# Performance work log

Measured on AMD Instinct MI355X. Metric: run time of the kernel, lower is better.

The kernel has to match this reference:

```python
import jax, jax.numpy as jnp
import numpy as np

B, R, C = 2, 64, 256
PH = PW = 7
KMAX = 8            # max pool-kernel size per axis given roi size bounds (kernel<=7 here)
HW = [160, 80, 40, 20]   # FPN level spatial sizes for a 640px image, strides 4/8/16/32
STRIDES = [4.0, 8.0, 16.0, 32.0]
TOP = 224.0         # config.top_pyramid_roi_size
HIDDEN = 2048
NCLS = 20
SCALE = float(np.round(np.sqrt(C), 2))  # np.round(sqrt(inner_dim),2) in SelfAttention


def setup_inputs() -> dict:
    key = jax.random.key(0)
    ks = jax.random.split(key, 32)
    U = lambda k, s, lo, hi: jax.random.uniform(k, s, minval=lo, maxval=hi)
    x1 = U(ks[0], (B, R), 0.0, 260.0)
    y1 = U(ks[1], (B, R), 0.0, 260.0)
    w = U(ks[2], (B, R), 16.0, 360.0)
    h = U(ks[3], (B, R), 16.0, 360.0)
    rois = jnp.stack([x1, y1, jnp.minimum(x1 + w, 639.0), jnp.minimum(y1 + h, 639.0)], -1)
    N = lambda k, s, sc: (sc * jax.random.normal(k, s)).astype(jnp.float32)
    inp = {'rois': rois}
    for i in range(4):
        inp[f'fm{i}'] = N(ks[4 + i], (B, C, HW[i], HW[i]), 1.0)
    inp['wq'] = N(ks[8], (C, C), 0.02);  inp['bq'] = jnp.zeros((C,), jnp.float32)
    inp['wk'] = N(ks[9], (C, C), 0.02);  inp['bk'] = jnp.zeros((C,), jnp.float32)
    inp['wv'] = N(ks[10], (C, C), 0.02); inp['bv'] = jnp.zeros((C,), jnp.float32)
    inp['wo'] = N(ks[11], (C, C), 0.02); inp['bo'] = jnp.zeros((C,), jnp.float32)
    inp['w1'] = N(ks[12], (C * PH * PW, HIDDEN), 0.02); inp['b1'] = jnp.zeros((HIDDEN,), jnp.float32)
    inp['w2'] = N(ks[13], (HIDDEN, HIDDEN), 0.02);       inp['b2'] = jnp.zeros((HIDDEN,), jnp.float32)
    inp['wreg'] = N(ks[14], (HIDDEN, 4 * (NCLS + 1)), 0.02); inp['breg'] = jnp.zeros((4 * (NCLS + 1),), jnp.float32)
    inp['wcls'] = N(ks[15], (HIDDEN, NCLS + 1), 0.02);       inp['bcls'] = jnp.zeros((NCLS + 1,), jnp.float32)
    return inp


def _forward(rois, fm0, fm1, fm2, fm3, wq, bq, wk, bk, wv, bv, wo, bo,
             w1, b1, w2, b2, wreg, breg, wcls, bcls):
    Hmax = HW[0]
    pad = lambda fm: jnp.pad(fm, ((0, 0), (0, 0), (0, Hmax - fm.shape[-2]), (0, Hmax - fm.shape[-1])))
    feats = jnp.stack([pad(fm0), pad(fm1), pad(fm2), pad(fm3)])  # [4,B,C,Hmax,Hmax]
    heights = jnp.array(HW, jnp.int32)
    strides = jnp.array(STRIDES, jnp.float32)

    r = rois.reshape(-1, 4)                 # [N,4] xyxy in pixels
    Nroi = r.shape[0]
    bidx = jnp.repeat(jnp.arange(B, dtype=jnp.int32), R)
    size = jnp.sqrt((r[:, 2] - r[:, 0]) * (r[:, 3] - r[:, 1]))
    # int() truncates toward zero, then clamp(0,3) -- matches torch
    lvl = jnp.clip((3.0 + jnp.log(size / TOP)).astype(jnp.int32), 0, 3)
    s = strides[lvl]
    x1 = (r[:, 0] / s).astype(jnp.int32); y1 = (r[:, 1] / s).astype(jnp.int32)
    x2 = (r[:, 2] / s).astype(jnp.int32); y2 = (r[:, 3] / s).astype(jnp.int32)
    Hl = heights[lvl]                        # per-roi level map size (square maps)

    def expand(lo, hi, cap, pool):
        # replicate the symmetric while-loop expansion until span >= pool
        for _ in range(pool):
            need = (hi - lo + 1) < pool
            lo = jnp.where(need, jnp.maximum(lo - 1, 0), lo)
            hi = jnp.where(need, jnp.minimum(hi + 1, cap - 1), hi)
        return lo, hi

    y1, y2 = expand(y1, y2, Hl, PH)
    x1, x2 = expand(x1, x2, Hl, PW)
    rh = y2 - y1 + 1; rw = x2 - x1 + 1
    kh = (rh + PH - 1) // PH; sh = rh // PH   # ceil / floor kernel & stride
    kw = (rw + PW - 1) // PW; sw = rw // PW

    ar_p = jnp.arange(PH); ar_k = jnp.arange(KMAX)

    def pool_one(l, b, yy, xx, kh_, kw_, sh_, sw_):
        rows = jnp.clip(yy + ar_p[:, None] * sh_ + ar_k[None, :], 0, Hmax - 1)  # [PH,K]
        cols = jnp.clip(xx + ar_p[:, None] * sw_ + ar_k[None, :], 0, Hmax - 1)  # [PW,K]
        patch = feats[l, b][:, rows[:, :, None, None], cols[None, None, :, :]]  # [C,PH,K,PW,K]
        m = (ar_k < kh_)[:, None, None] & (ar_k < kw_)[None, None, :]           # [K,1,K] -> bcast
        patch = jnp.where(m, patch, -jnp.inf)
        return patch.max(axis=(2, 4))                                           # [C,PH,PW]

    pooled = jax.vmap(pool_one)(lvl, bidx, y1, x1, kh, kw, sh, sw)  # [N,C,PH,PW]

    # SelfAttention over the PH*PW spatial tokens of each ROI
    L = PH * PW
    tok = pooled.reshape(Nroi, C, L).transpose(0, 2, 1)            # [N,L,C]
    q = tok @ wq + bq
    k = tok @ wk + bk
    v = tok @ wv + bv
    att = jax.nn.softmax(jnp.einsum('nlc,nmc->nlm', q, k) / SCALE, axis=-1)
    ctx = jnp.einsum('nlm,nmc->nlc', att, v) @ wo + bo             # [N,L,C]
    x = pooled.reshape(Nroi, C, L) + ctx.transpose(0, 2, 1)        # residual add
    x = x.reshape(Nroi, C * L)

    h1 = jax.nn.relu(x @ w1 + b1)
    h2 = jax.nn.relu(h1 @ w2 + b2)
    bbox_reg = h2 @ wreg + breg                                    # [N, 4*(NCLS+1)]
    bbox_classes = jax.nn.softmax(h2 @ wcls + bcls, axis=-1)       # [N, NCLS+1]
    return bbox_reg, bbox_classes


def reference(rois, fm0, fm1, fm2, fm3, wq, bq, wk, bk, wv, bv, wo, bo,
              w1, b1, w2, b2, wreg, breg, wcls, bcls):
    return _forward(rois, fm0, fm1, fm2, fm3, wq, bq, wk, bk, wv, bv, wo, bo,
                    w1, b1, w2, b2, wreg, breg, wcls, bcls)
```

## Files before the change

### kernel.cpp

```cpp
#include <hip/hip_runtime.h>
#include <hip/hip_bf16.h>
#include <stdint.h>

typedef __attribute__((ext_vector_type(8))) short bf16x8;
typedef __attribute__((ext_vector_type(4))) float f32x4;

__device__ __forceinline__ float blo(unsigned u){ union{float f;unsigned x;}v; v.x = u<<16; return v.f; }
__device__ __forceinline__ float bhi(unsigned u){ union{float f;unsigned x;}v; v.x = u & 0xFFFF0000u; return v.f; }
__device__ __forceinline__ unsigned short f2bf(float f){
  union{float f;unsigned x;}v; v.f=f; unsigned x=v.x;
  return (unsigned short)((x + 0x7fffu + ((x>>16)&1u)) >> 16);
}
__device__ __forceinline__ unsigned cvtpk(float lo, float hi){
  unsigned r;
  asm("v_cvt_pk_bf16_f32 %0, %1, %2" : "=v"(r) : "v"(lo), "v"(hi));
  return r;
}

__global__ __launch_bounds__(256) void pool_pack_kernel(
    const float* __restrict__ rois,
    const float* __restrict__ fm0, const float* __restrict__ fm1,
    const float* __restrict__ fm2, const float* __restrict__ fm3,
    float* __restrict__ pooled, unsigned short* __restrict__ tok,
    const float* __restrict__ wreg, const float* __restrict__ wcls, float* __restrict__ wT)
{
  int bx = blockIdx.x;
  int tid = threadIdx.x;
  if (bx >= 896){
    int c = bx - 896;
    if (c < 84){
      for (int k = tid; k < 2048; k += 256) wT[(size_t)c*2048 + k] = wreg[(size_t)k*84 + c];
    } else {
      int cc = c - 84;
      for (int k = tid; k < 2048; k += 256) wT[(size_t)c*2048 + k] = wcls[(size_t)k*21 + cc];
    }
    return;
  }
  int n = bx / 7;
  int ph = bx - n*7;
  int c = tid;
  const float* r = rois + n*4;
  int b = n >> 6;
  float rx1=r[0], ry1=r[1], rx2=r[2], ry2=r[3];
  float size = sqrtf((rx2-rx1)*(ry2-ry1));
  int lvl = (int)(3.0f + logf(size/224.0f));
  if (lvl < 0) lvl = 0; if (lvl > 3) lvl = 3;
  const float strides_[4] = {4.f,8.f,16.f,32.f};
  const int hw_[4] = {160,80,40,20};
  float s = strides_[lvl]; int Hl = hw_[lvl];
  int x1 = (int)(rx1/s), y1 = (int)(ry1/s), x2 = (int)(rx2/s), y2 = (int)(ry2/s);
  #pragma unroll
  for (int it=0; it<7; ++it){
    bool need = (y2-y1+1) < 7;
    if (need){ y1 = (y1-1 > 0) ? y1-1 : 0; y2 = (y2+1 < Hl-1) ? y2+1 : Hl-1; }
  }
  #pragma unroll
  for (int it=0; it<7; ++it){
    bool need = (x2-x1+1) < 7;
    if (need){ x1 = (x1-1 > 0) ? x1-1 : 0; x2 = (x2+1 < Hl-1) ? x2+1 : Hl-1; }
  }
  int rh = y2-y1+1, rw = x2-x1+1;
  int kh = (rh+6)/7, sh = rh/7, kw = (rw+6)/7, sw2 = rw/7;
  const float* fm = (lvl==0)?fm0:(lvl==1)?fm1:(lvl==2)?fm2:fm3;
  const float* fp = fm + ((size_t)(b*256 + c))*(size_t)(Hl*Hl);
  int r0 = y1 + ph*sh;
  for (int pw=0; pw<7; ++pw){
    int c0 = x1 + pw*sw2;
    float m = -3.4e38f;
    for (int i=0;i<kh;++i){
      const float* rp = fp + (size_t)(r0+i)*Hl + c0;
      for (int j=0;j<kw;++j) m = fmaxf(m, rp[j]);
    }
    int l = ph*7+pw;
    pooled[((size_t)n*49 + l)*256 + c] = m;
    tok[((size_t)n*49 + l)*256 + c] = f2bf(m);
  }
}

template<int EPI, int BSRC>
__global__ __launch_bounds__(256) void gemm_kernel(
    const unsigned short* __restrict__ A,
    const float* __restrict__ B0, const float* __restrict__ B1, const float* __restrict__ B2,
    const unsigned short* __restrict__ Bpre,
    const float* __restrict__ bias0, const float* __restrict__ bias1, const float* __restrict__ bias2,
    unsigned short* __restrict__ o0, unsigned short* __restrict__ o1, unsigned short* __restrict__ o2,
    float* __restrict__ outf, const float* __restrict__ pooled,
    int M, int Nper, int K, int nM, int nN, int kChunk,
    int nGemm, const float* __restrict__ convW, unsigned short* __restrict__ convP, int convMode)
{
  int tid = threadIdx.x;
  if ((int)blockIdx.x >= nGemm){
    int cb = blockIdx.x - nGemm;
    int wv = tid >> 6, lane = tid & 63;
    int krBase = lane >> 3;
    int bcgS = lane & 7;
    #pragma unroll
    for (int pass = 0; pass < 4; ++pass){
      int pr = cb*16 + pass*4 + wv;
      int k32 = pr >> 5, bn = pr & 31;
      uint4 vout0, vout1, vout2, vout3;
      #pragma unroll
      for (int q = 0; q < 4; ++q){
        int kr = krBase + (q<<3);
        int bcg = bcgS ^ ((kr>>3)<<1);
        int kp = k32*32 + kr;
        const float* srow;
        if (convMode == 1) srow = convW + ((size_t)((kp & 255)*49 + (kp >> 8)))*2048 + bn*64;
        else               srow = convW + (size_t)kp*2048 + bn*64;
        float4 a = *(const float4*)(srow + bcg*8);
        float4 b = *(const float4*)(srow + bcg*8 + 4);
        uint4 w;
        w.x = cvtpk(a.x,a.y); w.y = cvtpk(a.z,a.w);
        w.z = cvtpk(b.x,b.y); w.w = cvtpk(b.z,b.w);
        if (q==0) vout0 = w; else if (q==1) vout1 = w; else if (q==2) vout2 = w; else vout3 = w;
      }
      uint4* dst = (uint4*)(convP + (size_t)pr*2048);
      dst[lane      ] = vout0;
      dst[lane +  64] = vout1;
      dst[lane + 128] = vout2;
      dst[lane + 192] = vout3;
    }
    return;
  }

  __shared__ __align__(16) unsigned short Bs[2][2048];
  int per = nM*nN;
  int kc  = blockIdx.x / per;
  int rem = blockIdx.x - kc*per;
  int bm = rem % nM, bn = rem / nM;
  int m0 = bm*64, n0 = bn*64;
  int mat = n0 / Nper;
  int col0 = n0 - mat*Nper;
  const float* Bp    = (mat==0)?B0:(mat==1)?B1:B2;
  const float* biasp = (mat==0)?bias0:(mat==1)?bias1:bias2;
  unsigned short* outp = (mat==0)?o0:(mat==1)?o1:o2;
  int k0 = kc*kChunk;
  int nMacro = kChunk >> 7;
  int lane = tid & 63, wave = tid >> 6;
  int wm = wave & 1, wn = wave >> 1;
  int g = lane >> 4, c = lane & 15;

  f32x4 acc[2][2];
  #pragma unroll
  for (int i=0;i<2;++i)
    #pragma unroll
    for (int j=0;j<2;++j){ acc[i][j][0]=0.f; acc[i][j][1]=0.f; acc[i][j][2]=0.f; acc[i][j][3]=0.f; }

  int brow = tid >> 3, bcg = tid & 7;
  int bw_idx = brow*64 + ((bcg*8) ^ ((brow>>3)<<4));
  const float* Bbase = Bp + (size_t)brow*Nper + col0 + bcg*8;
  const unsigned short* Pbase = Bpre + (size_t)bn*2048 + tid*8;
  int rb0 = g*512 + (((wn*2  )^g)*16 + c);
  int rb1 = g*512 + (((wn*2+1)^g)*16 + c);
  const unsigned short* Ap0 = A + (size_t)(m0 + wm*32 +      c)*K + g*8;
  const unsigned short* Ap1 = A + (size_t)(m0 + wm*32 + 16 + c)*K + g*8;

  auto writeBf32 = [&](int buf, const float4& bx, const float4& by){
    uint4 w;
    w.x = cvtpk(bx.x,bx.y); w.y = cvtpk(bx.z,bx.w);
    w.z = cvtpk(by.x,by.y); w.w = cvtpk(by.z,by.w);
    *(uint4*)&Bs[buf][bw_idx] = w;
  };
  auto writeBpre = [&](int buf, const uint4& v){
    *(uint4*)&Bs[buf][tid*8] = v;
  };
  auto readFrags = [&](int buf, bf16x8& r0, bf16x8& r1){
    union { unsigned short s[8]; bf16x8 v; } u0, u1;
    const unsigned short* bsp = &Bs[buf][0];
    #pragma unroll
    for (int j=0;j<8;++j){ u0.s[j] = bsp[rb0 + j*64]; u1.s[j] = bsp[rb1 + j*64]; }
    r0 = u0.v; r1 = u1.v;
  };
  auto mfma4 = [&](const bf16x8& f0, const bf16x8& f1, const bf16x8& q0, const bf16x8& q1){
    acc[0][0] = __builtin_amdgcn_mfma_f32_16x16x32_bf16(f0,q0,acc[0][0],0,0,0);
    acc[0][1] = __builtin_amdgcn_mfma_f32_16x16x32_bf16(f0,q1,acc[0][1],0,0,0);
    acc[1][0] = __builtin_amdgcn_mfma_f32_16x16x32_bf16(f1,q0,acc[1][0],0,0,0);
    acc[1][1] = __builtin_amdgcn_mfma_f32_16x16x32_bf16(f1,q1,acc[1][1],0,0,0);
  };

  for (int mi = 0; mi < nMacro; ++mi){
    int kk = k0 + (mi << 7);
    uint4 a0x = *(const uint4*)(Ap0+kk),    a0y = *(const uint4*)(Ap1+kk);
    uint4 a1x = *(const uint4*)(Ap0+kk+32), a1y = *(const uint4*)(Ap1+kk+32);
    uint4 a2x = *(const uint4*)(Ap0+kk+64), a2y = *(const uint4*)(Ap1+kk+64);
    uint4 a3x = *(const uint4*)(Ap0+kk+96), a3y = *(const uint4*)(Ap1+kk+96);

    float4 b0a,b0b,b1a,b1b,b2a,b2b,b3a,b3b;
    uint4 v0,v1,v2,v3;
    if constexpr (BSRC==0){
      const float* p0 = Bbase + (size_t)kk*Nper;
      const float* p1 = p0 + (size_t)32*Nper;
      const float* p2 = p0 + (size_t)64*Nper;
      const float* p3 = p0 + (size_t)96*Nper;
      b0a = *(const float4*)p0; b0b = *(const float4*)(p0+4);
      b1a = *(const float4*)p1; b1b = *(const float4*)(p1+4);
      b2a = *(const float4*)p2; b2b = *(const float4*)(p2+4);
      b3a = *(const float4*)p3; b3b = *(const float4*)(p3+4);
    } else {
      const unsigned short* q = Pbase + (size_t)(kk>>5)*65536;
      v0 = *(const uint4*)q;
      v1 = *(const uint4*)(q + 65536);
      v2 = *(const uint4*)(q + 131072);
      v3 = *(const uint4*)(q + 196608);
    }

    if constexpr (BSRC==0) writeBf32(0,b0a,b0b); else writeBpre(0,v0);
    __syncthreads();

    bf16x8 q0,q1;
    readFrags(0,q0,q1);
    if constexpr (BSRC==0) writeBf32(1,b1a,b1b); else writeBpre(1,v1);
    mfma4(*(const bf16x8*)&a0x, *(const bf16x8*)&a0y, q0,q1);
    __syncthreads();

    readFrags(1,q0,q1);
    if constexpr (BSRC==0) writeBf32(0,b2a,b2b); else writeBpre(0,v2);
    mfma4(*(const bf16x8*)&a1x, *(const bf16x8*)&a1y, q0,q1);
    __syncthreads();

    readFrags(0,q0,q1);
    if constexpr (BSRC==0) writeBf32(1,b3a,b3b); else writeBpre(1,v3);
    mfma4(*(const bf16x8*)&a2x, *(const bf16x8*)&a2y, q0,q1);
    __syncthreads();

    readFrags(1,q0,q1);
    mfma4(*(const bf16x8*)&a3x, *(const bf16x8*)&a3y, q0,q1);
  }

  int rq = g << 2, cl = c;
  #pragma unroll
  for (int mr=0;mr<2;++mr){
    #pragma unroll
    for (int nc=0;nc<2;++nc){
      int rowb = m0 + wm*32 + mr*16 + rq;
      int colM = col0 + wn*32 + nc*16 + cl;
      #pragma unroll
      for (int r2=0;r2<4;++r2){
        float v = acc[mr][nc][r2];
        int rr = rowb + r2;
        if constexpr (EPI==0){
          v += biasp[colM];
          outp[(size_t)rr*Nper + colM] = f2bf(v);
        } else if constexpr (EPI==1){
          v += biasp[colM];
          v += pooled[(size_t)rr*256 + colM];
          int nn = rr/49, l = rr - nn*49;
          outp[(size_t)nn*12544 + l*256 + colM] = f2bf(v);
        } else {
          outf[(size_t)kc*M*Nper + (size_t)rr*Nper + colM] = v;
        }
      }
    }
  }
}

__global__ __launch_bounds__(256) void reduce1_kernel(
    const float* __restrict__ part, const float* __restrict__ b1,
    unsigned short* __restrict__ h1, int nPart)
{
  int i = blockIdx.x*256 + threadIdx.x;
  float4 s = ((const float4*)part)[i];
  for (int kc = 1; kc < nPart; ++kc){
    float4 p = ((const float4*)part)[(size_t)kc*65536 + i];
    s.x += p.x; s.y += p.y; s.z += p.z; s.w += p.w;
  }
  float4 bb = *(const float4*)(b1 + ((i<<2) & 2047));
  s.x = fmaxf(s.x+bb.x,0.f); s.y = fmaxf(s.y+bb.y,0.f);
  s.z = fmaxf(s.z+bb.z,0.f); s.w = fmaxf(s.w+bb.w,0.f);
  uint2 w;
  w.x = cvtpk(s.x, s.y); w.y = cvtpk(s.z, s.w);
  *(uint2*)&h1[(size_t)i<<2] = w;
}

__global__ __launch_bounds__(256) void reduce2_kernel(
    const float* __restrict__ part, float* __restrict__ h2f, int nPart)
{
  int i = blockIdx.x*256 + threadIdx.x;
  float4 s = ((const float4*)part)[i];
  for (int kc = 1; kc < nPart; ++kc){
    float4 p = ((const float4*)part)[(size_t)kc*65536 + i];
    s.x += p.x; s.y += p.y; s.z += p.z; s.w += p.w;
  }
  ((float4*)h2f)[i] = s;
}

__global__ __launch_bounds__(256) void attn_kernel(
    const unsigned short* __restrict__ Q, const unsigned short* __restrict__ Km,
    const unsigned short* __restrict__ V, unsigned short* __restrict__ ctx)
{
  int n = blockIdx.x, half = blockIdx.y, tid = threadIdx.x;
  int r0 = half*25, rcnt = half ? 24 : 25;
  __shared__ __align__(16) unsigned short qs[25*256];
  __shared__ __align__(16) unsigned short ks[49*260];
  __shared__ float S[25*49];
  const uint4* qg = (const uint4*)(Q + ((size_t)n*49 + r0)*256);
  for (int i = tid; i < rcnt*32; i += 256) ((uint4*)qs)[i] = qg[i];
  const uint2* kg = (const uint2*)(Km + (size_t)n*49*256);
  for (int i = tid; i < 49*64; i += 256){
    int j = i >> 6, s = i & 63;
    *(uint2*)(ks + j*260 + s*4) = kg[i];
  }
  __syncthreads();
  for (int p = tid; p < rcnt*49; p += 256){
    int i = p/49, j = p - i*49;
    const uint2* qr = (const uint2*)(qs + i*256);
    const uint2* kr = (const uint2*)(ks + j*260);
    float sum = 0.f;
    #pragma unroll 8
    for (int c4 = 0; c4 < 64; ++c4){
      uint2 qv = qr[c4], kv = kr[c4];
      sum += blo(qv.x)*blo(kv.x) + bhi(qv.x)*bhi(kv.x);
      sum += blo(qv.y)*blo(kv.y) + bhi(qv.y)*bhi(kv.y);
    }
    S[p] = sum * (1.0f/16.0f);
  }
  __syncthreads();
  const uint2* vg = (const uint2*)(V + (size_t)n*49*256);
  for (int i = tid; i < 49*64; i += 256){
    int j = i >> 6, s = i & 63;
    *(uint2*)(ks + j*260 + s*4) = vg[i];
  }
  if (tid < rcnt){
    float* row = S + tid*49;
    float mx = row[0];
    for (int j=1;j<49;++j) mx = fmaxf(mx,row[j]);
    float sm = 0.f;
    for (int j=0;j<49;++j){ float e = expf(row[j]-mx); row[j]=e; sm+=e; }
    float inv = 1.0f/sm;
    for (int j=0;j<49;++j) row[j] *= inv;
  }
  __syncthreads();
  for (int idx = tid; idx < rcnt*64; idx += 256){
    int i = idx >> 6, cp4 = idx & 63;
    const float* att = S + i*49;
    float s0=0.f, s1=0.f, s2=0.f, s3=0.f;
    #pragma unroll 7
    for (int j=0;j<49;++j){
      uint2 v = *(const uint2*)(ks + j*260 + cp4*4);
      float a = att[j];
      s0 += a*blo(v.x); s1 += a*bhi(v.x);
      s2 += a*blo(v.y); s3 += a*bhi(v.y);
    }
    uint2 outw;
    outw.x = (unsigned)f2bf(s0) | ((unsigned)f2bf(s1) << 16);
    outw.y = (unsigned)f2bf(s2) | ((unsigned)f2bf(s3) << 16);
    *(uint2*)&ctx[((size_t)n*49 + r0 + i)*256 + cp4*4] = outw;
  }
}

__global__ __launch_bounds__(256) void heads_dot(
    const float* __restrict__ h2f, const float* __restrict__ b2,
    const float* __restrict__ wT,
    const float* __restrict__ breg, const float* __restrict__ bcls,
    float* __restrict__ out, float* __restrict__ logits)
{
  int gw = (blockIdx.x*256 + threadIdx.x) >> 6;
  int lane = threadIdx.x & 63;
  int m = gw / 105, c = gw - m*105;
  const float4* hp = (const float4*)(h2f + (size_t)m*2048);
  const float4* bp = (const float4*)b2;
  const float4* wp = (const float4*)(wT + (size_t)c*2048);
  float sum = 0.f;
  #pragma unroll
  for (int i=0;i<8;++i){
    float4 a = hp[i*64 + lane];
    float4 bb = bp[i*64 + lane];
    float4 w = wp[i*64 + lane];
    sum += fmaxf(a.x+bb.x,0.f)*w.x + fmaxf(a.y+bb.y,0.f)*w.y
         + fmaxf(a.z+bb.z,0.f)*w.z + fmaxf(a.w+bb.w,0.f)*w.w;
  }
  #pragma unroll
  for (int off=32; off; off>>=1) sum += __shfl_down(sum, off, 64);
  if (lane == 0){
    if (c < 84) out[(size_t)m*84 + c] = sum + breg[c];
    else        logits[(size_t)m*21 + (c-84)] = sum + bcls[c-84];
  }
}

__global__ __launch_bounds__(128) void cls_softmax(
    const float* __restrict__ logits, float* __restrict__ out)
{
  int m = threadIdx.x;
  const float* lg = logits + (size_t)m*21;
  float mx = lg[0];
  #pragma unroll
  for (int j=1;j<21;++j) mx = fmaxf(mx, lg[j]);
  float sm = 0.f;
  float e[21];
  #pragma unroll
  for (int j=0;j<21;++j){ e[j] = expf(lg[j]-mx); sm += e[j]; }
  float inv = 1.0f/sm;
  #pragma unroll
  for (int j=0;j<21;++j) out[10752 + (size_t)m*21 + j] = e[j]*inv;
}

extern "C" void kernel_launch(void* const* d_in, const int* in_sizes, int n_in,
                              void* d_out, int out_size, void* d_ws, size_t ws_size,
                              hipStream_t stream)
{
  (void)in_sizes; (void)n_in; (void)out_size; (void)ws_size;
  const float* rois = (const float*)d_in[0];
  const float* fm0  = (const float*)d_in[1];
  const float* fm1  = (const float*)d_in[2];
  const float* fm2  = (const float*)d_in[3];
  const float* fm3  = (const float*)d_in[4];
  const float* wq   = (const float*)d_in[5];
  const float* bq   = (const float*)d_in[6];
  const float* wk   = (const float*)d_in[7];
  const float* bk   = (const float*)d_in[8];
  const float* wv   = (const float*)d_in[9];
  const float* bv   = (const float*)d_in[10];
  const float* wo   = (const float*)d_in[11];
  const float* bo   = (const float*)d_in[12];
  const float* w1   = (const float*)d_in[13];
  const float* b1   = (const float*)d_in[14];
  const float* w2   = (const float*)d_in[15];
  const float* b2   = (const float*)d_in[16];
  const float* wreg = (const float*)d_in[17];
  const float* breg = (const float*)d_in[18];
  const float* wcls = (const float*)d_in[19];
  const float* bcls = (const float*)d_in[20];
  float* out = (float*)d_out;

  char* ws = (char*)d_ws;
  float*          pooled = (float*)(ws + 0);
  unsigned short* tok    = (unsigned short*)(ws + 6422528);
  unsigned short* Qb     = (unsigned short*)(ws + 9633792);
  unsigned short* Kb     = (unsigned short*)(ws + 12845056);
  unsigned short* Vb     = (unsigned short*)(ws + 16056320);
  unsigned short* ctx    = (unsigned short*)(ws + 19267584);
  unsigned short* xb     = (unsigned short*)(ws + 22478848);
  float*          h2f    = (float*)(ws + 25690112);
  unsigned short* h1     = (unsigned short*)(ws + 26738688);
  float*          wT     = (float*)(ws + 27787264);
  float*          logits = (float*)(ws + 28647424);
  unsigned short* w1p    = (unsigned short*)(ws + 29360128);
  unsigned short* w2p    = (unsigned short*)(ws + 80740352);
  float*          h1part = (float*)(ws + 0);
  float*          h2part = (float*)(ws + 0);

  pool_pack_kernel<<<1001,256,0,stream>>>(rois, fm0, fm1, fm2, fm3, pooled, tok,
                                          wreg, wcls, wT);

  gemm_kernel<0,0><<<1176+784,256,0,stream>>>(tok, wq,wk,wv, nullptr, bq,bk,bv,
                                              Qb,Kb,Vb, nullptr, nullptr,
                                              6272,256,256, 98,12, 256,
                                              1176, w1, w1p, 1);

  attn_kernel<<<dim3(128,2),256,0,stream>>>(Qb, Kb, Vb, ctx);

  gemm_kernel<1,0><<<392+128,256,0,stream>>>(ctx, wo,wo,wo, nullptr, bo,bo,bo,
                                             xb,xb,xb, nullptr, pooled,
                                             6272,256,256, 98,4, 256,
                                             392, w2, w2p, 2);

  gemm_kernel<2,1><<<896,256,0,stream>>>(xb, nullptr,nullptr,nullptr, w1p,
                                         nullptr,nullptr,nullptr, nullptr,nullptr,nullptr,
                                         h1part, nullptr, 128,2048,12544, 2,32, 896,
                                         896, nullptr, nullptr, 0);
  reduce1_kernel<<<256,256,0,stream>>>(h1part, b1, h1, 14);

  gemm_kernel<2,1><<<1024,256,0,stream>>>(h1, nullptr,nullptr,nullptr, w2p,
                                          nullptr,nullptr,nullptr, nullptr,nullptr,nullptr,
                                          h2part, nullptr, 128,2048,2048, 2,32, 128,
                                          1024, nullptr, nullptr, 0);
  reduce2_kernel<<<256,256,0,stream>>>(h2part, h2f, 16);

  heads_dot<<<3360,256,0,stream>>>(h2f, b2, wT, breg, bcls, out, logits);
  cls_softmax<<<1,128,0,stream>>>(logits, out);
}
```

Before: 178.1 us.

## Store residual activations channel-major and remap GEMM blocks across XCDs

The pooled buffer and the residual output xb now use channel-major [n][c][l] order, matching the C*49 flattening that w1 expects. This lets the w1 pre-pack read rows contiguously instead of through the permuted (k&255)*49+(k>>8) gather. The two large split-K GEMMs also remap block IDs so that consecutive logical tiles land on the same XCD, aiming for better L2 reuse of the packed weights. The cost is strided, poorly coalesced bf16 stores in the wo epilogue and strided pooled writes in the pooling kernel.

Result: slower. 212.5 us (+19.3%).

```diff
diff --git a/kernel.cpp b/kernel.cpp
--- a/kernel.cpp
+++ b/kernel.cpp
@@ -72,12 +72,12 @@
       for (int j=0;j<kw;++j) m = fmaxf(m, rp[j]);
     }
     int l = ph*7+pw;
-    pooled[((size_t)n*49 + l)*256 + c] = m;
+    pooled[((size_t)n*256 + c)*49 + l] = m;
     tok[((size_t)n*49 + l)*256 + c] = f2bf(m);
   }
 }
 
-template<int EPI, int BSRC>
+template<int EPI, int BSRC, bool XCDR>
 __global__ __launch_bounds__(256) void gemm_kernel(
     const unsigned short* __restrict__ A,
     const float* __restrict__ B0, const float* __restrict__ B1, const float* __restrict__ B2,
@@ -86,7 +86,7 @@
     unsigned short* __restrict__ o0, unsigned short* __restrict__ o1, unsigned short* __restrict__ o2,
     float* __restrict__ outf, const float* __restrict__ pooled,
     int M, int Nper, int K, int nM, int nN, int kChunk,
-    int nGemm, const float* __restrict__ convW, unsigned short* __restrict__ convP, int convMode)
+    int nGemm, const float* __restrict__ convW, unsigned short* __restrict__ convP)
 {
   int tid = threadIdx.x;
   if ((int)blockIdx.x >= nGemm){
@@ -103,10 +103,7 @@
       for (int q = 0; q < 4; ++q){
         int kr = krBase + (q<<3);
         int bcg = bcgS ^ ((kr>>3)<<1);
-        int kp = k32*32 + kr;
-        const float* srow;
-        if (convMode == 1) srow = convW + ((size_t)((kp & 255)*49 + (kp >> 8)))*2048 + bn*64;
-        else               srow = convW + (size_t)kp*2048 + bn*64;
+        const float* srow = convW + (size_t)(k32*32 + kr)*2048 + bn*64;
         float4 a = *(const float4*)(srow + bcg*8);
         float4 b = *(const float4*)(srow + bcg*8 + 4);
         uint4 w;
@@ -124,9 +121,14 @@
   }
 
   __shared__ __align__(16) unsigned short Bs[2][2048];
+  int bid = blockIdx.x;
+  if constexpr (XCDR){
+    int pe = gridDim.x >> 3;
+    bid = (bid & 7)*pe + (bid >> 3);
+  }
   int per = nM*nN;
-  int kc  = blockIdx.x / per;
-  int rem = blockIdx.x - kc*per;
+  int kc  = bid / per;
+  int rem = bid - kc*per;
   int bm = rem % nM, bn = rem / nM;
   int m0 = bm*64, n0 = bn*64;
   int mat = n0 / Nper;
@@ -243,9 +245,9 @@
           outp[(size_t)rr*Nper + colM] = f2bf(v);
         } else if constexpr (EPI==1){
           v += biasp[colM];
-          v += pooled[(size_t)rr*256 + colM];
           int nn = rr/49, l = rr - nn*49;
-          outp[(size_t)nn*12544 + l*256 + colM] = f2bf(v);
+          v += pooled[((size_t)nn*256 + colM)*49 + l];
+          outp[(size_t)nn*12544 + colM*49 + l] = f2bf(v);
         } else {
           outf[(size_t)kc*M*Nper + (size_t)rr*Nper + colM] = v;
         }
@@ -442,28 +444,28 @@
   pool_pack_kernel<<<1001,256,0,stream>>>(rois, fm0, fm1, fm2, fm3, pooled, tok,
                                           wreg, wcls, wT);
 
-  gemm_kernel<0,0><<<1176+784,256,0,stream>>>(tok, wq,wk,wv, nullptr, bq,bk,bv,
-                                              Qb,Kb,Vb, nullptr, nullptr,
-                                              6272,256,256, 98,12, 256,
-                                              1176, w1, w1p, 1);
+  gemm_kernel<0,0,false><<<1176+784,256,0,stream>>>(tok, wq,wk,wv, nullptr, bq,bk,bv,
+                                                    Qb,Kb,Vb, nullptr, nullptr,
+                                                    6272,256,256, 98,12, 256,
+                                                    1176, w1, w1p);
 
   attn_kernel<<<dim3(128,2),256,0,stream>>>(Qb, Kb, Vb, ctx);
 
-  gemm_kernel<1,0><<<392+128,256,0,stream>>>(ctx, wo,wo,wo, nullptr, bo,bo,bo,
-                                             xb,xb,xb, nullptr, pooled,
-                                             6272,256,256, 98,4, 256,
-                                             392, w2, w2p, 2);
-
-  gemm_kernel<2,1><<<896,256,0,stream>>>(xb, nullptr,nullptr,nullptr, w1p,
-                                         nullptr,nullptr,nullptr, nullptr,nullptr,nullptr,
-                                         h1part, nullptr, 128,2048,12544, 2,32, 896,
-                                         896, nullptr, nullptr, 0);
+  gemm_kernel<1,0,false><<<392+128,256,0,stream>>>(ctx, wo,wo,wo, nullptr, bo,bo,bo,
+                                                   xb,xb,xb, nullptr, pooled,
+                                                   6272,256,256, 98,4, 256,
+                                                   392, w2, w2p);
+
+  gemm_kernel<2,1,true><<<896,256,0,stream>>>(xb, nullptr,nullptr,nullptr, w1p,
+                                              nullptr,nullptr,nullptr, nullptr,nullptr,nullptr,
+                                              h1part, nullptr, 128,2048,12544, 2,32, 896,
+                                              896, nullptr, nullptr);
   reduce1_kernel<<<256,256,0,stream>>>(h1part, b1, h1, 14);
 
-  gemm_kernel<2,1><<<1024,256,0,stream>>>(h1, nullptr,nullptr,nullptr, w2p,
-                                          nullptr,nullptr,nullptr, nullptr,nullptr,nullptr,
-                                          h2part, nullptr, 128,2048,2048, 2,32, 128,
-                                          1024, nullptr, nullptr, 0);
+  gemm_kernel<2,1,true><<<1024,256,0,stream>>>(h1, nullptr,nullptr,nullptr, w2p,
+                                               nullptr,nullptr,nullptr, nullptr,nullptr,nullptr,
+                                               h2part, nullptr, 128,2048,2048, 2,32, 128,
+                                               1024, nullptr, nullptr);
   reduce2_kernel<<<256,256,0,stream>>>(h2part, h2f, 16);
 
   heads_dot<<<3360,256,0,stream>>>(h2f, b2, wT, breg, bcls, out, logits);
```
